# Kernel tuning notes

Measured on AMD Instinct MI355X. Metric: run time of the kernel, lower is better.

## Reference

```python
import jax, jax.numpy as jnp
import numpy as np

T, B, H, L = 512, 64, 100, 10  # seq_len, batch, hidden, num_layers


def setup_inputs() -> dict:
    key = jax.random.key(0)
    ks = jax.random.split(key, 8)
    s = 0.1  # ~ PyTorch uniform(-1/sqrt(H), 1/sqrt(H)) scale
    return {
        "x": jax.random.normal(ks[0], (T, B, H), jnp.float32),
        "W_ih0": jax.random.normal(ks[1], (2, H, H), jnp.float32) * s,
        "W_ih": jax.random.normal(ks[2], (L - 1, 2, H, 2 * H), jnp.float32) * s,
        "W_hh": jax.random.normal(ks[3], (L, 2, H, H), jnp.float32) * s,
        "b_ih": jax.random.normal(ks[4], (L, 2, H), jnp.float32) * s,
        "b_hh": jax.random.normal(ks[5], (L, 2, H), jnp.float32) * s,
        "W_out": jax.random.normal(ks[6], (1, 2 * H), jnp.float32) * s,
        "b_out": jax.random.normal(ks[7], (1,), jnp.float32) * s,
    }


def _rnn_dir(x, Wih, Whh, b, reverse):
    # Precompute input projection for all timesteps as one big GEMM.
    # z: [T, B, H]; b already holds b_ih + b_hh.
    z = jnp.einsum('tbi,hi->tbh', x, Wih) + b
    h0 = jnp.zeros((x.shape[1], Whh.shape[0]), x.dtype)

    def step(h, zt):
        h = jnp.tanh(zt + h @ Whh.T)
        return h, h

    # reverse=True scans backward in time but emits outputs in original order,
    # exactly matching the backward direction of a bidirectional RNN.
    _, ys = jax.lax.scan(step, h0, z, reverse=reverse)
    return ys  # [T, B, H]


def reference(x, W_ih0, W_ih, W_hh, b_ih, b_hh, W_out, b_out):
    h = x
    for l in range(L):
        Wih_l = W_ih0 if l == 0 else W_ih[l - 1]
        fwd = _rnn_dir(h, Wih_l[0], W_hh[l, 0], b_ih[l, 0] + b_hh[l, 0], False)
        bwd = _rnn_dir(h, Wih_l[1], W_hh[l, 1], b_ih[l, 1] + b_hh[l, 1], True)
        h = jnp.concatenate([fwd, bwd], axis=-1)  # [T, B, 2H]
    y = jax.nn.sigmoid(jnp.einsum('tbh,oh->tbo', h, W_out) + b_out)  # [T, B, 1]
    return y.reshape(-1)  # [T*B]
```

## Files before the change

### kernel.cpp

```cpp
#include <hip/hip_runtime.h>
#include <math.h>


#define T_LEN 512
#define BATCH 64
#define HID   100
#define M_TOT (T_LEN * BATCH)

__global__ __launch_bounds__(256) void ingemm_kernel(
    const float* __restrict__ In, const float* __restrict__ W,
    const float* __restrict__ bih, const float* __restrict__ bhh,
    float* __restrict__ z, int K)
{
    __shared__ float As[16][132];
    __shared__ float Bs[16][68];
    const int tid = threadIdx.x;
    const int m0 = blockIdx.x * 128;
    const int n0 = blockIdx.y * 64;
    const int tx = tid & 15, ty = tid >> 4;
    const int lm = tid >> 2;
    const int lk = (tid & 3) << 2;

    float acc[8][4];
    #pragma unroll
    for (int i = 0; i < 8; ++i)
        #pragma unroll
        for (int j = 0; j < 4; ++j) acc[i][j] = 0.f;

    for (int k0 = 0; k0 < K; k0 += 16) {
        #pragma unroll
        for (int rep = 0; rep < 2; ++rep) {
            float4 av = make_float4(0.f,0.f,0.f,0.f);
            const int row = lm + 64 * rep;
            if (k0 + lk < K)
                av = *(const float4*)(In + (size_t)(m0 + row) * K + k0 + lk);
            As[lk+0][row]=av.x; As[lk+1][row]=av.y;
            As[lk+2][row]=av.z; As[lk+3][row]=av.w;
        }
        {
            float4 bv = make_float4(0.f,0.f,0.f,0.f);
            const int nrow = n0 + lm;
            if (nrow < 200 && k0 + lk < K)
                bv = *(const float4*)(W + (size_t)nrow * K + k0 + lk);
            Bs[lk+0][lm]=bv.x; Bs[lk+1][lm]=bv.y;
            Bs[lk+2][lm]=bv.z; Bs[lk+3][lm]=bv.w;
        }
        __syncthreads();
        #pragma unroll
        for (int kk = 0; kk < 16; ++kk) {
            float4 alo = *(const float4*)&As[kk][ty << 2];
            float4 ahi = *(const float4*)&As[kk][64 + (ty << 2)];
            float4 b4  = *(const float4*)&Bs[kk][tx << 2];
            float a[8] = {alo.x, alo.y, alo.z, alo.w,
                          ahi.x, ahi.y, ahi.z, ahi.w};
            float b[4] = {b4.x, b4.y, b4.z, b4.w};
            #pragma unroll
            for (int i = 0; i < 8; ++i)
                #pragma unroll
                for (int j = 0; j < 4; ++j)
                    acc[i][j] += a[i] * b[j];
        }
        __syncthreads();
    }
    #pragma unroll
    for (int i = 0; i < 8; ++i) {
        const int m = m0 + ((i < 4) ? ((ty << 2) + i) : (64 + (ty << 2) + (i - 4)));
        #pragma unroll
        for (int j = 0; j < 4; ++j) {
            const int n = n0 + (tx << 2) + j;
            if (n < 200) {
                const int dir = (n >= 100) ? 1 : 0;
                const int h = n - dir * 100;
                z[(size_t)dir * M_TOT * HID + (size_t)m * HID + h] =
                    acc[i][j] + bih[n] + bhh[n];
            }
        }
    }
}

__device__ __forceinline__ float dpp_qxor1(float x) {
    int i = __float_as_int(x);
    i = __builtin_amdgcn_update_dpp(0, i, 0xB1, 0xF, 0xF, false);
    return __int_as_float(i);
}
__device__ __forceinline__ float dpp_qxor2(float x) {
    int i = __float_as_int(x);
    i = __builtin_amdgcn_update_dpp(0, i, 0x4E, 0xF, 0xF, false);
    return __int_as_float(i);
}
__device__ __forceinline__ float dpp_hmir(float x) {
    int i = __float_as_int(x);
    i = __builtin_amdgcn_update_dpp(0, i, 0x141, 0xF, 0xF, false);
    return __int_as_float(i);
}

__global__ __launch_bounds__(256) void scan_kernel(
    const float* __restrict__ z,
    const float* __restrict__ Whh,
    float* __restrict__ out)
{
    const int dir = blockIdx.x >> 6;
    const int b   = blockIdx.x & 63;
    const int tid = threadIdx.x;
    const int w   = tid >> 6;
    const int lane= tid & 63;
    const int q   = lane & 3;
    const int b2  = (lane >> 2) & 1;
    const int ks  = q | (b2 << 2);
    const int slot= (lane >> 3) + 8 * w;
    const bool active = (slot < 25);
    const int slotc = active ? slot : 24;
    const int jout = 4 * slotc + q;
    const bool writer = active && (b2 == 0);
    const int kb = 12 * ks;

    __shared__ float h_lds[2][112];
    for (int i = tid; i < 224; i += 256) (&h_lds[0][0])[i] = 0.f;

    float w4[4][16];
    #pragma unroll
    for (int r = 0; r < 4; ++r) {
        const float* wr = Whh + ((size_t)dir * HID + 4 * slotc + r) * HID + kb;
        #pragma unroll
        for (int i = 0; i < 4; ++i) {
            float4 v = *(const float4*)(wr + 4 * i);
            w4[r][4*i+0] = v.x; w4[r][4*i+1] = v.y;
            w4[r][4*i+2] = v.z; w4[r][4*i+3] = v.w;
        }
        if (ks > 0) {
            w4[r][0] = 0.f; w4[r][1] = 0.f; w4[r][2] = 0.f; w4[r][3] = 0.f;
        }
    }
    __syncthreads();

    const ptrdiff_t zstride = BATCH * HID;
    const ptrdiff_t ostride = BATCH * 200;
    const int t0 = dir ? (T_LEN - 1) : 0;
    const ptrdiff_t zstep = dir ? -zstride : zstride;
    const ptrdiff_t ostep = dir ? -ostride : ostride;
    const ptrdiff_t zstep2 = 2 * zstep, zstep3 = 3 * zstep, zstep4 = 4 * zstep;

    const float* zp = z + (size_t)dir * M_TOT * HID + (size_t)b * HID + jout
                        + (ptrdiff_t)t0 * zstride;
    float*       op = out + (size_t)b * 200 + dir * HID + jout
                        + (ptrdiff_t)t0 * ostride;

    float zr0 = zp[0];
    float zr1 = zp[zstep];
    float zr2 = zp[zstep2];
    float zr3 = zp[zstep3];
    const float* zpf = zp + zstep4;

#define RNN_STEP(ZREG, DO_PF, PFOFF, RD, WRB)                           \
  do {                                                                  \
    const float zin = ZREG;                                             \
    if (DO_PF) ZREG = *(zpf + (PFOFF));   \
    const float4* hp = (const float4*)((RD) + kb);                      \
    float a0 = 0.f, a1 = 0.f, a2 = 0.f, a3 = 0.f;                       \
    _Pragma("unroll")                                                   \
    for (int i = 0; i < 4; ++i) {                                       \
      float4 hv = hp[i];                                                \
      a0 += w4[0][4*i+0] * hv.x; a0 += w4[0][4*i+1] * hv.y;             \
      a0 += w4[0][4*i+2] * hv.z; a0 += w4[0][4*i+3] * hv.w;             \
      a1 += w4[1][4*i+0] * hv.x; a1 += w4[1][4*i+1] * hv.y;             \
      a1 += w4[1][4*i+2] * hv.z; a1 += w4[1][4*i+3] * hv.w;             \
      a2 += w4[2][4*i+0] * hv.x; a2 += w4[2][4*i+1] * hv.y;             \
      a2 += w4[2][4*i+2] * hv.z; a2 += w4[2][4*i+3] * hv.w;             \
      a3 += w4[3][4*i+0] * hv.x; a3 += w4[3][4*i+1] * hv.y;             \
      a3 += w4[3][4*i+2] * hv.z; a3 += w4[3][4*i+3] * hv.w;             \
    }                                                                   \
           \
    float t0_ = a0 + dpp_hmir(a0);                                      \
    float t1_ = a1 + dpp_hmir(a1);                                      \
    float t2_ = a2 + dpp_hmir(a2);                                      \
    float t3_ = a3 + dpp_hmir(a3);                                      \
                                     \
    float k01 = (q & 1) ? t1_ : t0_;                                    \
    float s01s = (q & 1) ? t0_ : t1_;                                   \
    float s01 = k01 + dpp_qxor1(s01s);                                  \
    float k23 = (q & 1) ? t3_ : t2_;                                    \
    float s23s = (q & 1) ? t2_ : t3_;                                   \
    float s23 = k23 + dpp_qxor1(s23s);                                  \
        \
    float kf = (q & 2) ? s23 : s01;                                     \
    float sf = (q & 2) ? s01 : s23;                                     \
    float tot = kf + dpp_qxor2(sf);                                     \
    float xin = zin + tot;                                              \
    float ax = fabsf(xin);                                              \
    float e = __expf(2.f * ax);                                         \
    float r = 1.f - 2.f / (e + 1.f);                                    \
    float val = copysignf(r, xin);                                      \
    if (writer) {                                                       \
      (WRB)[jout] = val;                                                \
      *op = val;                                                        \
    }                                                                   \
    op += ostep;                                                        \
    asm volatile("s_waitcnt lgkmcnt(0)" ::: "memory");                  \
    __builtin_amdgcn_sched_barrier(0);                                  \
    __builtin_amdgcn_s_barrier();                                       \
    __builtin_amdgcn_sched_barrier(0);                                  \
  } while (0)

    float* const h0 = &h_lds[0][0];
    float* const h1 = &h_lds[1][0];

    for (int g = 0; g < (T_LEN / 4) - 1; ++g) {
        RNN_STEP(zr0, 1, 0,      h0, h1);
        RNN_STEP(zr1, 1, zstep,  h1, h0);
        RNN_STEP(zr2, 1, zstep2, h0, h1);
        RNN_STEP(zr3, 1, zstep3, h1, h0);
        zpf += zstep4;
    }
    RNN_STEP(zr0, 0, 0, h0, h1);
    RNN_STEP(zr1, 0, 0, h1, h0);
    RNN_STEP(zr2, 0, 0, h0, h1);
    RNN_STEP(zr3, 0, 0, h1, h0);

#undef RNN_STEP
}

__global__ __launch_bounds__(256) void outproj_kernel(
    const float* __restrict__ h, const float* __restrict__ Wout,
    const float* __restrict__ bout, float* __restrict__ y)
{
    const int gid = blockIdx.x * 256 + threadIdx.x;
    const int wid = gid >> 6;
    const int lane = threadIdx.x & 63;
    if (wid >= M_TOT) return;
    const float* row = h + (size_t)wid * 200;
    float acc = 0.f;
    for (int k = lane; k < 200; k += 64) acc += row[k] * Wout[k];
    #pragma unroll
    for (int off = 32; off > 0; off >>= 1) acc += __shfl_xor(acc, off);
    if (lane == 0) y[wid] = 1.f / (1.f + __expf(-(acc + bout[0])));
}

extern "C" void kernel_launch(void* const* d_in, const int* in_sizes, int n_in,
                              void* d_out, int out_size, void* d_ws, size_t ws_size,
                              hipStream_t stream)
{
    const float* x     = (const float*)d_in[0];
    const float* W_ih0 = (const float*)d_in[1];
    const float* W_ih  = (const float*)d_in[2];
    const float* W_hh  = (const float*)d_in[3];
    const float* b_ih  = (const float*)d_in[4];
    const float* b_hh  = (const float*)d_in[5];
    const float* W_out = (const float*)d_in[6];
    const float* b_out = (const float*)d_in[7];
    float* y = (float*)d_out;

    float* z    = (float*)d_ws;
    float* buf0 = z + (size_t)2 * M_TOT * HID;
    float* buf1 = buf0 + (size_t)M_TOT * 200;

    for (int l = 0; l < 10; ++l) {
        const float* In = (l == 0) ? x : ((l & 1) ? buf0 : buf1);
        float* Out      = (l & 1) ? buf1 : buf0;
        const int K     = (l == 0) ? 100 : 200;
        const float* W  = (l == 0) ? W_ih0 : (W_ih + (size_t)(l - 1) * 2 * 100 * 200);
        ingemm_kernel<<<dim3(M_TOT / 128, 4), 256, 0, stream>>>(
            In, W, b_ih + l * 200, b_hh + l * 200, z, K);
        scan_kernel<<<128, 256, 0, stream>>>(
            z, W_hh + (size_t)l * 2 * HID * HID, Out);
    }
    outproj_kernel<<<M_TOT / 4, 256, 0, stream>>>(buf1, W_out, b_out, y);
}
```

Before: 2.204 ms.

## Use split-bf16 MFMA for layer input GEMMs with padded bf16 hidden buffers

The scan kernel now writes hidden states as hi/lo bf16 pairs into K-padded (224) buffers. Layers 1-9 compute the input projection with a new MFMA 16x16x32 bf16 kernel that uses three products (hi*hi, hi*lo, lo*hi) to approximate fp32 accuracy. Per-layer weight splitting and a one-time zero-pad kernel are added, while layer 0 keeps the fp32 SIMT GEMM. This is meant to cut input-GEMM time on matrix cores, at the cost of extra conversion work in the serial scan, two extra launches per layer, and a small loss of precision.

Result: faster. 2.110 ms (-4.3%).

```diff
diff --git a/kernel.cpp b/kernel.cpp
--- a/kernel.cpp
+++ b/kernel.cpp
@@ -6,6 +6,12 @@
 #define BATCH 64
 #define HID   100
 #define M_TOT (T_LEN * BATCH)
+#define KPAD  224
+#define NPAD  208
+
+typedef unsigned short ushort_t;
+typedef __attribute__((ext_vector_type(8))) __bf16 bf16x8;
+typedef __attribute__((ext_vector_type(4))) float f32x4;
 
 __global__ __launch_bounds__(256) void ingemm_kernel(
     const float* __restrict__ In, const float* __restrict__ W,
@@ -78,6 +84,85 @@
     }
 }
 
+__device__ __forceinline__ unsigned bf16_rne(float v) {
+    unsigned u = __float_as_uint(v);
+    return (u + 0x7FFFu + ((u >> 16) & 1u)) >> 16;
+}
+
+__global__ __launch_bounds__(256) void zeropad_kernel(
+    ushort_t* a, ushort_t* b, ushort_t* c, ushort_t* d)
+{
+    int i = blockIdx.x * 256 + threadIdx.x;
+    if (i >= M_TOT * 24) return;
+    size_t off = (size_t)(i / 24) * KPAD + 200 + (i % 24);
+    a[off] = 0; b[off] = 0; c[off] = 0; d[off] = 0;
+}
+
+__global__ __launch_bounds__(256) void wsplit_kernel(
+    const float* __restrict__ W, ushort_t* __restrict__ whi,
+    ushort_t* __restrict__ wlo)
+{
+    int i = blockIdx.x * 256 + threadIdx.x;
+    if (i >= NPAD * KPAD) return;
+    int n = i / KPAD, k = i % KPAD;
+    float v = (n < 200 && k < 200) ? W[n * 200 + k] : 0.f;
+    unsigned hr = bf16_rne(v);
+    float hv = __uint_as_float(hr << 16);
+    unsigned lr = bf16_rne(v - hv);
+    whi[i] = (ushort_t)hr;
+    wlo[i] = (ushort_t)lr;
+}
+
+__global__ __launch_bounds__(256) void ingemm_mfma_kernel(
+    const ushort_t* __restrict__ in_hi, const ushort_t* __restrict__ in_lo,
+    const ushort_t* __restrict__ w_hi,  const ushort_t* __restrict__ w_lo,
+    const float* __restrict__ bih, const float* __restrict__ bhh,
+    float* __restrict__ z)
+{
+    const int wv   = threadIdx.x >> 6;
+    const int lane = threadIdx.x & 63;
+    const int mt   = blockIdx.x * 4 + wv;
+    const int m0   = mt * 16;
+    const int r16  = lane & 15;
+    const int kg   = lane >> 4;
+    const int kof  = kg * 8;
+
+    bf16x8 ah[7], al[7];
+    const ushort_t* arh = in_hi + (size_t)(m0 + r16) * KPAD + kof;
+    const ushort_t* arl = in_lo + (size_t)(m0 + r16) * KPAD + kof;
+    #pragma unroll
+    for (int c = 0; c < 7; ++c) {
+        ah[c] = *(const bf16x8*)(arh + 32 * c);
+        al[c] = *(const bf16x8*)(arl + 32 * c);
+    }
+
+    for (int nt = 0; nt < 13; ++nt) {
+        const int n0 = nt * 16;
+        const ushort_t* brh = w_hi + (size_t)(n0 + r16) * KPAD + kof;
+        const ushort_t* brl = w_lo + (size_t)(n0 + r16) * KPAD + kof;
+        f32x4 acc = {0.f, 0.f, 0.f, 0.f};
+        #pragma unroll
+        for (int c = 0; c < 7; ++c) {
+            bf16x8 bh = *(const bf16x8*)(brh + 32 * c);
+            bf16x8 bl = *(const bf16x8*)(brl + 32 * c);
+            acc = __builtin_amdgcn_mfma_f32_16x16x32_bf16(ah[c], bh, acc, 0, 0, 0);
+            acc = __builtin_amdgcn_mfma_f32_16x16x32_bf16(ah[c], bl, acc, 0, 0, 0);
+            acc = __builtin_amdgcn_mfma_f32_16x16x32_bf16(al[c], bh, acc, 0, 0, 0);
+        }
+        const int n = n0 + r16;
+        if (n < 200) {
+            const int dir = (n >= 100) ? 1 : 0;
+            const int h = n - dir * 100;
+            const float bias = bih[n] + bhh[n];
+            #pragma unroll
+            for (int r = 0; r < 4; ++r) {
+                const int m = m0 + kg * 4 + r;
+                z[(size_t)dir * M_TOT * HID + (size_t)m * HID + h] = acc[r] + bias;
+            }
+        }
+    }
+}
+
 __device__ __forceinline__ float dpp_qxor1(float x) {
     int i = __float_as_int(x);
     i = __builtin_amdgcn_update_dpp(0, i, 0xB1, 0xF, 0xF, false);
@@ -97,7 +182,8 @@
 __global__ __launch_bounds__(256) void scan_kernel(
     const float* __restrict__ z,
     const float* __restrict__ Whh,
-    float* __restrict__ out)
+    ushort_t* __restrict__ ohi,
+    ushort_t* __restrict__ olo)
 {
     const int dir = blockIdx.x >> 6;
     const int b   = blockIdx.x & 63;
@@ -134,7 +220,7 @@
     __syncthreads();
 
     const ptrdiff_t zstride = BATCH * HID;
-    const ptrdiff_t ostride = BATCH * 200;
+    const ptrdiff_t ostride = BATCH * KPAD;
     const int t0 = dir ? (T_LEN - 1) : 0;
     const ptrdiff_t zstep = dir ? -zstride : zstride;
     const ptrdiff_t ostep = dir ? -ostride : ostride;
@@ -142,8 +228,8 @@
 
     const float* zp = z + (size_t)dir * M_TOT * HID + (size_t)b * HID + jout
                         + (ptrdiff_t)t0 * zstride;
-    float*       op = out + (size_t)b * 200 + dir * HID + jout
-                        + (ptrdiff_t)t0 * ostride;
+    ushort_t* oph = ohi + ((size_t)t0 * BATCH + b) * KPAD + dir * HID + jout;
+    ushort_t* opl = olo + ((size_t)t0 * BATCH + b) * KPAD + dir * HID + jout;
 
     float zr0 = zp[0];
     float zr1 = zp[zstep];
@@ -154,7 +240,7 @@
 #define RNN_STEP(ZREG, DO_PF, PFOFF, RD, WRB)                           \
   do {                                                                  \
     const float zin = ZREG;                                             \
-    if (DO_PF) ZREG = *(zpf + (PFOFF));   \
+    if (DO_PF) ZREG = *(zpf + (PFOFF));                                 \
     const float4* hp = (const float4*)((RD) + kb);                      \
     float a0 = 0.f, a1 = 0.f, a2 = 0.f, a3 = 0.f;                       \
     _Pragma("unroll")                                                   \
@@ -169,19 +255,16 @@
       a3 += w4[3][4*i+0] * hv.x; a3 += w4[3][4*i+1] * hv.y;             \
       a3 += w4[3][4*i+2] * hv.z; a3 += w4[3][4*i+3] * hv.w;             \
     }                                                                   \
-           \
     float t0_ = a0 + dpp_hmir(a0);                                      \
     float t1_ = a1 + dpp_hmir(a1);                                      \
     float t2_ = a2 + dpp_hmir(a2);                                      \
     float t3_ = a3 + dpp_hmir(a3);                                      \
-                                     \
     float k01 = (q & 1) ? t1_ : t0_;                                    \
     float s01s = (q & 1) ? t0_ : t1_;                                   \
     float s01 = k01 + dpp_qxor1(s01s);                                  \
     float k23 = (q & 1) ? t3_ : t2_;                                    \
     float s23s = (q & 1) ? t2_ : t3_;                                   \
     float s23 = k23 + dpp_qxor1(s23s);                                  \
-        \
     float kf = (q & 2) ? s23 : s01;                                     \
     float sf = (q & 2) ? s01 : s23;                                     \
     float tot = kf + dpp_qxor2(sf);                                     \
@@ -192,9 +275,13 @@
     float val = copysignf(r, xin);                                      \
     if (writer) {                                                       \
       (WRB)[jout] = val;                                                \
-      *op = val;                                                        \
+      unsigned hr = bf16_rne(val);                                      \
+      float hv2 = __uint_as_float(hr << 16);                            \
+      unsigned lr = bf16_rne(val - hv2);                                \
+      *oph = (ushort_t)hr;                                              \
+      *opl = (ushort_t)lr;                                              \
     }                                                                   \
-    op += ostep;                                                        \
+    oph += ostep; opl += ostep;                                         \
     asm volatile("s_waitcnt lgkmcnt(0)" ::: "memory");                  \
     __builtin_amdgcn_sched_barrier(0);                                  \
     __builtin_amdgcn_s_barrier();                                       \
@@ -220,16 +307,22 @@
 }
 
 __global__ __launch_bounds__(256) void outproj_kernel(
-    const float* __restrict__ h, const float* __restrict__ Wout,
-    const float* __restrict__ bout, float* __restrict__ y)
+    const ushort_t* __restrict__ hh, const ushort_t* __restrict__ hl,
+    const float* __restrict__ Wout, const float* __restrict__ bout,
+    float* __restrict__ y)
 {
     const int gid = blockIdx.x * 256 + threadIdx.x;
     const int wid = gid >> 6;
     const int lane = threadIdx.x & 63;
     if (wid >= M_TOT) return;
-    const float* row = h + (size_t)wid * 200;
+    const ushort_t* rh = hh + (size_t)wid * KPAD;
+    const ushort_t* rl = hl + (size_t)wid * KPAD;
     float acc = 0.f;
-    for (int k = lane; k < 200; k += 64) acc += row[k] * Wout[k];
+    for (int k = lane; k < 200; k += 64) {
+        float hv = __uint_as_float((unsigned)rh[k] << 16)
+                 + __uint_as_float((unsigned)rl[k] << 16);
+        acc += hv * Wout[k];
+    }
     #pragma unroll
     for (int off = 32; off > 0; off >>= 1) acc += __shfl_xor(acc, off);
     if (lane == 0) y[wid] = 1.f / (1.f + __expf(-(acc + bout[0])));
@@ -249,19 +342,31 @@
     const float* b_out = (const float*)d_in[7];
     float* y = (float*)d_out;
 
-    float* z    = (float*)d_ws;
-    float* buf0 = z + (size_t)2 * M_TOT * HID;
-    float* buf1 = buf0 + (size_t)M_TOT * 200;
-
-    for (int l = 0; l < 10; ++l) {
-        const float* In = (l == 0) ? x : ((l & 1) ? buf0 : buf1);
-        float* Out      = (l & 1) ? buf1 : buf0;
-        const int K     = (l == 0) ? 100 : 200;
-        const float* W  = (l == 0) ? W_ih0 : (W_ih + (size_t)(l - 1) * 2 * 100 * 200);
-        ingemm_kernel<<<dim3(M_TOT / 128, 4), 256, 0, stream>>>(
-            In, W, b_ih + l * 200, b_hh + l * 200, z, K);
+    float* z = (float*)d_ws;
+    ushort_t* hiA = (ushort_t*)(z + (size_t)2 * M_TOT * HID);
+    ushort_t* loA = hiA + (size_t)M_TOT * KPAD;
+    ushort_t* hiB = loA + (size_t)M_TOT * KPAD;
+    ushort_t* loB = hiB + (size_t)M_TOT * KPAD;
+    ushort_t* whi = loB + (size_t)M_TOT * KPAD;
+    ushort_t* wlo = whi + (size_t)NPAD * KPAD;
+
+    zeropad_kernel<<<(M_TOT * 24 + 255) / 256, 256, 0, stream>>>(hiA, loA, hiB, loB);
+
+    ingemm_kernel<<<dim3(M_TOT / 128, 4), 256, 0, stream>>>(
+        x, W_ih0, b_ih, b_hh, z, 100);
+    scan_kernel<<<128, 256, 0, stream>>>(z, W_hh, hiA, loA);
+
+    for (int l = 1; l < 10; ++l) {
+        const ushort_t* ih = (l & 1) ? hiA : hiB;
+        const ushort_t* il = (l & 1) ? loA : loB;
+        ushort_t* oh = (l & 1) ? hiB : hiA;
+        ushort_t* ol = (l & 1) ? loB : loA;
+        wsplit_kernel<<<(NPAD * KPAD + 255) / 256, 256, 0, stream>>>(
+            W_ih + (size_t)(l - 1) * 2 * 100 * 200, whi, wlo);
+        ingemm_mfma_kernel<<<512, 256, 0, stream>>>(
+            ih, il, whi, wlo, b_ih + l * 200, b_hh + l * 200, z);
         scan_kernel<<<128, 256, 0, stream>>>(
-            z, W_hh + (size_t)l * 2 * HID * HID, Out);
-    }
-    outproj_kernel<<<M_TOT / 4, 256, 0, stream>>>(buf1, W_out, b_out, y);
-}
+            z, W_hh + (size_t)l * 2 * HID * HID, oh, ol);
+    }
+    outproj_kernel<<<M_TOT / 4, 256, 0, stream>>>(hiB, loB, W_out, b_out, y);
+}
```
